# Performance work log

Measured on AMD Instinct MI355X. Metric: run time of the kernel, lower is better.

The kernel has to match this reference:

```python
import jax, jax.numpy as jnp
import numpy as np

N_NODES = 50000
N_EDGES = 300000
F_IN, HID, N_CLS = 256, 256, 128


def _glorot_linear(key, fan_in, fan_out):
    # torch.nn.Linear-style uniform init, kaiming bound 1/sqrt(fan_in)
    s = 1.0 / np.sqrt(fan_in)
    return jax.random.uniform(key, (fan_in, fan_out), jnp.float32, -s, s)


def setup_inputs() -> dict:
    key = jax.random.key(0)
    ks = jax.random.split(key, 8)
    x = jax.random.normal(ks[0], (N_NODES, F_IN), jnp.float32)
    edge_index = jax.random.randint(ks[1], (2, N_EDGES), 0, N_NODES, dtype=jnp.int32)
    return {
        "x": x,
        "edge_index": edge_index,
        "W1": _glorot_linear(ks[2], F_IN, HID), "b1": jnp.zeros((HID,), jnp.float32),
        "W2": _glorot_linear(ks[3], HID, HID),  "b2": jnp.zeros((HID,), jnp.float32),
        "W3": _glorot_linear(ks[4], HID, HID),  "b3": jnp.zeros((HID,), jnp.float32),
        "W4": _glorot_linear(ks[5], HID, N_CLS), "b4": jnp.zeros((N_CLS,), jnp.float32),
    }


def _gcn_conv(x, W, b, src, dst, norm, n):
    # x' = D^{-1/2} (A + I) D^{-1/2} X W + b   (PyG GCNConv default)
    h = x @ W                                  # [N, out]
    msg = h[src] * norm[:, None]               # gather + edge scaling  [E', out]
    return jax.ops.segment_sum(msg, dst, num_segments=n) + b


def reference(x, edge_index, W1, b1, W2, b2, W3, b3, W4, b4):
    n = x.shape[0]
    loops = jnp.arange(n, dtype=edge_index.dtype)
    src = jnp.concatenate([edge_index[0], loops])  # add self-loops
    dst = jnp.concatenate([edge_index[1], loops])
    # symmetric normalization: deg over target nodes (unit edge weights)
    deg = jax.ops.segment_sum(jnp.ones_like(dst, jnp.float32), dst, num_segments=n)
    dis = jnp.where(deg > 0, jax.lax.rsqrt(jnp.maximum(deg, 1.0)), 0.0)
    norm = dis[src] * dis[dst]                     # [E']

    h = jax.nn.relu(_gcn_conv(x, W1, b1, src, dst, norm, n))
    h = jax.nn.relu(_gcn_conv(h, W2, b2, src, dst, norm, n))
    h = jax.nn.relu(_gcn_conv(h, W3, b3, src, dst, norm, n))
    h = _gcn_conv(h, W4, b4, src, dst, norm, n)    # [N, C]

    # global_add_pool with batch == zeros -> single-graph sum pool
    pooled = jnp.sum(h, axis=0, keepdims=True)     # [1, C]
    return (pooled, jax.nn.log_softmax(pooled, axis=1))
```

## Files before the change

### kernel.cpp

```cpp
#include <hip/hip_runtime.h>


typedef __attribute__((ext_vector_type(8))) short short8;
typedef __attribute__((ext_vector_type(8))) signed char schar8;
typedef __attribute__((ext_vector_type(4))) float float4v;

__device__ __forceinline__ unsigned short f2b(float f) {
    unsigned int u = __builtin_bit_cast(unsigned int, f);
    u += 0x7fffu + ((u >> 16) & 1u);
    return (unsigned short)(u >> 16);
}
__device__ __forceinline__ float b2f(unsigned short b) {
    unsigned int u = ((unsigned int)b) << 16;
    return __builtin_bit_cast(float, u);
}

__global__ void zero_convert_kernel(int* __restrict__ cnt, float* __restrict__ tsum,
                                    float* __restrict__ accbuf,
                                    const float* __restrict__ W1, const float* __restrict__ W2,
                                    const float* __restrict__ W3, unsigned short* __restrict__ Wt1,
                                    unsigned short* __restrict__ Wt2, unsigned short* __restrict__ Wt3,
                                    const float* __restrict__ x, unsigned short* __restrict__ xb,
                                    int N, int nb) {
    int t = threadIdx.x;
    int b = blockIdx.x;
    if (b < nb) {
        int i = b * 256 + t;
        if (i < N) { cnt[i] = 0; tsum[i] = 0.f; }
        if (b == 0) accbuf[t] = 0.f;
    } else if (b < nb + 768) {
        int bb = b - nb;
        int w = bb >> 8;
        int n = bb & 255;
        const float* W = (w == 0) ? W1 : (w == 1) ? W2 : W3;
        unsigned short* Wt = (w == 0) ? Wt1 : (w == 1) ? Wt2 : Wt3;
        Wt[n * 256 + t] = f2b(W[t * 256 + n]);
    } else {
        size_t base = ((size_t)(b - nb - 768) * 256 + t) * 8;
        if (base < (size_t)N * 256) {
            float4 lo = *(const float4*)&x[base];
            float4 hi = *(const float4*)&x[base + 4];
            uint4 o;
            o.x = (unsigned int)f2b(lo.x) | ((unsigned int)f2b(lo.y) << 16);
            o.y = (unsigned int)f2b(lo.z) | ((unsigned int)f2b(lo.w) << 16);
            o.z = (unsigned int)f2b(hi.x) | ((unsigned int)f2b(hi.y) << 16);
            o.w = (unsigned int)f2b(hi.z) | ((unsigned int)f2b(hi.w) << 16);
            *(uint4*)&xb[base] = o;
        }
    }
}

__global__ void count_kernel(const int* __restrict__ dst, int* __restrict__ cnt, int E) {
    int i = blockIdx.x * blockDim.x + threadIdx.x;
    if (i < E) atomicAdd(&cnt[dst[i]], 1);
}

__global__ void blocksum_kernel(const int* __restrict__ cnt, int* __restrict__ bsum, int N) {
    __shared__ int s[256];
    int t = threadIdx.x;
    int i = blockIdx.x * 256 + t;
    s[t] = (i < N) ? cnt[i] : 0;
    __syncthreads();
    for (int d = 128; d > 0; d >>= 1) {
        if (t < d) s[t] += s[t + d];
        __syncthreads();
    }
    if (t == 0) bsum[blockIdx.x] = s[0];
}

__global__ void finalize_kernel(const int* __restrict__ cnt, const int* __restrict__ bsum,
                                int* __restrict__ offs, int* __restrict__ cursor,
                                float* __restrict__ dis, int N, int E, int nb) {
    __shared__ int bs[256];
    __shared__ int s[256];
    int t = threadIdx.x;
    bs[t] = (t < nb) ? bsum[t] : 0;
    __syncthreads();
    for (int d = 1; d < 256; d <<= 1) {
        int x = (t >= d) ? bs[t - d] : 0;
        __syncthreads();
        bs[t] += x;
        __syncthreads();
    }
    int blockoff = (blockIdx.x == 0) ? 0 : bs[blockIdx.x - 1];
    int i = blockIdx.x * 256 + t;
    int c = (i < N) ? cnt[i] : 0;
    s[t] = c;
    __syncthreads();
    for (int d = 1; d < 256; d <<= 1) {
        int x = (t >= d) ? s[t - d] : 0;
        __syncthreads();
        s[t] += x;
        __syncthreads();
    }
    if (i < N) {
        int ex = blockoff + s[t] - c;
        offs[i] = ex;
        cursor[i] = ex;
        dis[i] = rsqrtf((float)(c + 1));
    }
    if (blockIdx.x == 0 && t == 0) offs[N] = E;
}

__global__ void scatter_outsum_kernel(const int* __restrict__ src, const int* __restrict__ dst,
                                      const float* __restrict__ dis, int* __restrict__ cursor,
                                      int* __restrict__ csr_src, float* __restrict__ csr_nrm,
                                      float* __restrict__ tsum, int E) {
    int i = blockIdx.x * blockDim.x + threadIdx.x;
    if (i < E) {
        int s = src[i], d = dst[i];
        float dd = dis[d];
        int pos = atomicAdd(&cursor[d], 1);
        csr_src[pos] = s;
        csr_nrm[pos] = dis[s] * dd;
        atomicAdd(&tsum[s], dd);
    }
}

__global__ __launch_bounds__(256, 5) void gemm_bf16_kernel(
        const unsigned short* __restrict__ Ab, const unsigned short* __restrict__ Wt,
        signed char* __restrict__ C8, float* __restrict__ Ts, int M) {
    __shared__ unsigned short As[64 * 64];
    __shared__ unsigned short Bs[128 * 64];
    const int tid = threadIdx.x;
    const int lane = tid & 63;
    const int wave = tid >> 6;
    const int l15 = lane & 15;
    const int quad = lane >> 4;
    const int wm = wave & 1;
    const int wn = wave >> 1;

    const int bid = blockIdx.x;
    const int grp = bid >> 4;
    const int ii = bid & 15;
    const int xv = grp * 8 + (ii & 7);
    const int yv = ii >> 3;
    const int m0 = xv * 64;
    const int n0 = yv * 128;
    if (m0 >= M) return;

    float4v acc[2][4] = {};

    const int lrow = lane >> 3;
    const int lslot = (lane & 7) ^ lrow;

    const unsigned short* Bt = Wt + (size_t)n0 * 256;

    for (int kk = 0; kk < 256; kk += 64) {
#pragma unroll
        for (int i = 0; i < 2; i++) {
            int r0 = wave * 16 + i * 8;
            int gm = m0 + r0 + lrow;
            if (gm >= M) gm = M - 1;
            const unsigned short* gp = &Ab[(size_t)gm * 256 + kk + lslot * 8];
            __builtin_amdgcn_global_load_lds(
                (const __attribute__((address_space(1))) unsigned int*)gp,
                (__attribute__((address_space(3))) unsigned int*)&As[r0 * 64],
                16, 0, 0);
        }
#pragma unroll
        for (int i = 0; i < 4; i++) {
            int r0 = wave * 32 + i * 8;
            const unsigned short* gp = &Bt[(size_t)(r0 + lrow) * 256 + kk + lslot * 8];
            __builtin_amdgcn_global_load_lds(
                (const __attribute__((address_space(1))) unsigned int*)gp,
                (__attribute__((address_space(3))) unsigned int*)&Bs[r0 * 64],
                16, 0, 0);
        }
        __syncthreads();
#pragma unroll
        for (int ks = 0; ks < 64; ks += 32) {
            const int sl = (ks >> 3) + quad;
            short8 af[2], bf[4];
#pragma unroll
            for (int mi = 0; mi < 2; mi++) {
                int row = wm * 32 + mi * 16 + l15;
                af[mi] = *(const short8*)&As[row * 64 + 8 * (sl ^ (row & 7))];
            }
#pragma unroll
            for (int nj = 0; nj < 4; nj++) {
                int row = wn * 64 + nj * 16 + l15;
                bf[nj] = *(const short8*)&Bs[row * 64 + 8 * (sl ^ (row & 7))];
            }
#pragma unroll
            for (int mi = 0; mi < 2; mi++)
#pragma unroll
                for (int nj = 0; nj < 4; nj++)
                    acc[mi][nj] = __builtin_amdgcn_mfma_f32_16x16x32_bf16(
                        af[mi], bf[nj], acc[mi][nj], 0, 0, 0);
        }
        __syncthreads();
    }

    float* pmax = (float*)As;
    float* pinv = (float*)&As[512];
#pragma unroll
    for (int mi = 0; mi < 2; mi++) {
#pragma unroll
        for (int r = 0; r < 4; r++) {
            float m = fabsf(acc[mi][0][r]);
            m = fmaxf(m, fabsf(acc[mi][1][r]));
            m = fmaxf(m, fabsf(acc[mi][2][r]));
            m = fmaxf(m, fabsf(acc[mi][3][r]));
            m = fmaxf(m, __shfl_xor(m, 1));
            m = fmaxf(m, __shfl_xor(m, 2));
            m = fmaxf(m, __shfl_xor(m, 4));
            m = fmaxf(m, __shfl_xor(m, 8));
            if (l15 == 0) pmax[(wm * 32 + mi * 16 + quad * 4 + r) * 2 + wn] = m;
        }
    }
    __syncthreads();
    if (tid < 64) {
        float m = fmaxf(pmax[tid * 2], pmax[tid * 2 + 1]);
        int grow = m0 + tid;
        if (grow < M) Ts[(size_t)grow * 2 + yv] = m * (1.f / 127.f);
        pinv[tid] = (m > 0.f) ? 127.f / m : 0.f;
    }
    __syncthreads();
#pragma unroll
    for (int mi = 0; mi < 2; mi++) {
#pragma unroll
        for (int r = 0; r < 4; r++) {
            int lr = wm * 32 + mi * 16 + quad * 4 + r;
            float inv = pinv[lr];
            int row = m0 + lr;
            if (row < M) {
#pragma unroll
                for (int nj = 0; nj < 4; nj++) {
                    int col = n0 + wn * 64 + nj * 16 + l15;
                    C8[(size_t)row * 256 + col] =
                        (signed char)__float2int_rn(acc[mi][nj][r] * inv);
                }
            }
        }
    }
}

template <int RELU>
__global__ __launch_bounds__(256) void agg_bf16_kernel(
        const signed char* __restrict__ T8, const float* __restrict__ Ts,
        const float* __restrict__ bias,
        const int* __restrict__ offs, const int* __restrict__ csr_src,
        const float* __restrict__ csr_nrm, const float* __restrict__ dis,
        unsigned short* __restrict__ out, int N) {
    int hw = threadIdx.x >> 5;
    int l = threadIdx.x & 31;
    int v = blockIdx.x * 8 + hw;
    if (v >= N) return;
    int f8 = l * 8;
    int hh = l >> 4;
    int beg = offs[v], end = offs[v + 1];
    float dv = dis[v];
    float w = dv * dv * Ts[(size_t)v * 2 + hh];
    float a[8];
    {
        schar8 q = *(const schar8*)&T8[(size_t)v * 256 + f8];
#pragma unroll
        for (int i = 0; i < 8; i++) a[i] = w * (float)q[i];
    }
    int e = beg;
    for (; e + 4 <= end; e += 4) {
        int s0 = csr_src[e],     s1 = csr_src[e + 1];
        int s2 = csr_src[e + 2], s3 = csr_src[e + 3];
        float n0 = csr_nrm[e]     * Ts[(size_t)s0 * 2 + hh];
        float n1 = csr_nrm[e + 1] * Ts[(size_t)s1 * 2 + hh];
        float n2 = csr_nrm[e + 2] * Ts[(size_t)s2 * 2 + hh];
        float n3 = csr_nrm[e + 3] * Ts[(size_t)s3 * 2 + hh];
        schar8 h0 = *(const schar8*)&T8[(size_t)s0 * 256 + f8];
        schar8 h1 = *(const schar8*)&T8[(size_t)s1 * 256 + f8];
        schar8 h2 = *(const schar8*)&T8[(size_t)s2 * 256 + f8];
        schar8 h3 = *(const schar8*)&T8[(size_t)s3 * 256 + f8];
#pragma unroll
        for (int i = 0; i < 8; i++)
            a[i] += n0 * (float)h0[i] + n1 * (float)h1[i]
                  + n2 * (float)h2[i] + n3 * (float)h3[i];
    }
    for (; e < end; e++) {
        int s = csr_src[e];
        float nm = csr_nrm[e] * Ts[(size_t)s * 2 + hh];
        schar8 h = *(const schar8*)&T8[(size_t)s * 256 + f8];
#pragma unroll
        for (int i = 0; i < 8; i++) a[i] += nm * (float)h[i];
    }
    float4 bv0 = *(const float4*)&bias[f8];
    float4 bv1 = *(const float4*)&bias[f8 + 4];
    a[0] += bv0.x; a[1] += bv0.y; a[2] += bv0.z; a[3] += bv0.w;
    a[4] += bv1.x; a[5] += bv1.y; a[6] += bv1.z; a[7] += bv1.w;
    if (RELU) {
#pragma unroll
        for (int i = 0; i < 8; i++) a[i] = fmaxf(a[i], 0.f);
    }
    uint4 o;
    o.x = (unsigned int)f2b(a[0]) | ((unsigned int)f2b(a[1]) << 16);
    o.y = (unsigned int)f2b(a[2]) | ((unsigned int)f2b(a[3]) << 16);
    o.z = (unsigned int)f2b(a[4]) | ((unsigned int)f2b(a[5]) << 16);
    o.w = (unsigned int)f2b(a[6]) | ((unsigned int)f2b(a[7]) << 16);
    *(uint4*)&out[(size_t)v * 256 + f8] = o;
}

__global__ __launch_bounds__(256) void wpool_partial(
        const unsigned short* __restrict__ H, const float* __restrict__ dis,
        const float* __restrict__ tsum, float* __restrict__ partial, int N) {
    int tid = threadIdx.x;
    int f8 = (tid & 31) * 8;
    int rg = tid >> 5;
    float a[8] = {};
    for (int r = blockIdx.x * 8 + rg; r < N; r += gridDim.x * 8) {
        float s = dis[r] * (dis[r] + tsum[r]);
        short8 h = *(const short8*)&H[(size_t)r * 256 + f8];
#pragma unroll
        for (int i = 0; i < 8; i++) a[i] += s * b2f((unsigned short)h[i]);
    }
    __shared__ float red[8 * 256];
#pragma unroll
    for (int i = 0; i < 8; i++) red[rg * 256 + f8 + i] = a[i];
    __syncthreads();
    for (int s = 4; s > 0; s >>= 1) {
        if (rg < s) {
#pragma unroll
            for (int i = 0; i < 8; i++)
                red[rg * 256 + f8 + i] += red[(rg + s) * 256 + f8 + i];
        }
        __syncthreads();
    }
    partial[(size_t)blockIdx.x * 256 + tid] = red[tid];
}

__global__ void wpool_reduce(const float* __restrict__ partial, float* __restrict__ acc) {
    int f = threadIdx.x;
    int p0 = blockIdx.x * 32;
    float a = 0.f;
#pragma unroll
    for (int p = 0; p < 32; p++) a += partial[(size_t)(p0 + p) * 256 + f];
    atomicAdd(&acc[f], a);
}

__global__ void final_kernel(const float* __restrict__ acc, const float* __restrict__ W4,
                             const float* __restrict__ b4, float* __restrict__ out, int N) {
    __shared__ float red[128];
    int c = threadIdx.x;
    float p = (float)N * b4[c];
    for (int k = 0; k < 256; k++) p += acc[k] * W4[k * 128 + c];
    out[c] = p;
    red[c] = p;
    __syncthreads();
    for (int s = 64; s > 0; s >>= 1) {
        if (c < s) red[c] = fmaxf(red[c], red[c + s]);
        __syncthreads();
    }
    float m = red[0];
    __syncthreads();
    red[c] = expf(p - m);
    __syncthreads();
    for (int s = 64; s > 0; s >>= 1) {
        if (c < s) red[c] += red[c + s];
        __syncthreads();
    }
    float lse = m + logf(red[0]);
    out[128 + c] = p - lse;
}

extern "C" void kernel_launch(void* const* d_in, const int* in_sizes, int n_in,
                              void* d_out, int out_size, void* d_ws, size_t ws_size,
                              hipStream_t stream) {
    const float* x  = (const float*)d_in[0];
    const int*   ei = (const int*)d_in[1];
    const float* W1 = (const float*)d_in[2];
    const float* b1 = (const float*)d_in[3];
    const float* W2 = (const float*)d_in[4];
    const float* b2 = (const float*)d_in[5];
    const float* W3 = (const float*)d_in[6];
    const float* b3 = (const float*)d_in[7];
    const float* W4 = (const float*)d_in[8];
    const float* b4 = (const float*)d_in[9];

    const int N = in_sizes[0] / 256;
    const int E = in_sizes[1] / 2;
    const int* src = ei;
    const int* dst = ei + E;

    char* p = (char*)d_ws;
    auto alloc = [&](size_t bytes) {
        char* r = p;
        p += (bytes + 255) & ~(size_t)255;
        return r;
    };
    int*            cnt     = (int*)alloc((size_t)N * 4);
    int*            offs    = (int*)alloc((size_t)(N + 1) * 4);
    int*            cursor  = (int*)alloc((size_t)N * 4);
    float*          dis     = (float*)alloc((size_t)N * 4);
    float*          tsum    = (float*)alloc((size_t)N * 4);
    int*            bsum    = (int*)alloc(1024 * 4);
    int*            csr_src = (int*)alloc((size_t)E * 4);
    float*          csr_nrm = (float*)alloc((size_t)E * 4);
    unsigned short* Wt1     = (unsigned short*)alloc(256 * 256 * 2);
    unsigned short* Wt2     = (unsigned short*)alloc(256 * 256 * 2);
    unsigned short* Wt3     = (unsigned short*)alloc(256 * 256 * 2);
    unsigned short* xb      = (unsigned short*)alloc((size_t)N * 256 * 2);
    signed char*    T8      = (signed char*)alloc((size_t)N * 256);
    float*          Ts      = (float*)alloc((size_t)N * 2 * 4);
    unsigned short* Abuf    = (unsigned short*)alloc((size_t)N * 256 * 2);
    float*          partial = (float*)alloc((size_t)1024 * 256 * 4);
    float*          accbuf  = (float*)alloc(256 * 4);

    int eb = (E + 255) / 256;
    int nb = (N + 255) / 256;
    int ncvt = (N * 32 + 255) / 256;
    zero_convert_kernel<<<nb + 768 + ncvt, 256, 0, stream>>>(
        cnt, tsum, accbuf, W1, W2, W3, Wt1, Wt2, Wt3, x, xb, N, nb);
    count_kernel<<<eb, 256, 0, stream>>>(dst, cnt, E);
    blocksum_kernel<<<nb, 256, 0, stream>>>(cnt, bsum, N);
    finalize_kernel<<<nb, 256, 0, stream>>>(cnt, bsum, offs, cursor, dis, N, E, nb);
    scatter_outsum_kernel<<<eb, 256, 0, stream>>>(src, dst, dis, cursor, csr_src,
                                                  csr_nrm, tsum, E);

    int mtiles = (N + 63) / 64;
    int ggrid = ((mtiles + 7) / 8) * 16;
    int ab = (N + 7) / 8;
    gemm_bf16_kernel<<<ggrid, 256, 0, stream>>>(xb, Wt1, T8, Ts, N);
    agg_bf16_kernel<1><<<ab, 256, 0, stream>>>(T8, Ts, b1, offs, csr_src, csr_nrm, dis, Abuf, N);
    gemm_bf16_kernel<<<ggrid, 256, 0, stream>>>(Abuf, Wt2, T8, Ts, N);
    agg_bf16_kernel<1><<<ab, 256, 0, stream>>>(T8, Ts, b2, offs, csr_src, csr_nrm, dis, Abuf, N);
    gemm_bf16_kernel<<<ggrid, 256, 0, stream>>>(Abuf, Wt3, T8, Ts, N);
    agg_bf16_kernel<1><<<ab, 256, 0, stream>>>(T8, Ts, b3, offs, csr_src, csr_nrm, dis, Abuf, N);

    wpool_partial<<<1024, 256, 0, stream>>>(Abuf, dis, tsum, partial, N);
    wpool_reduce<<<32, 256, 0, stream>>>(partial, accbuf);
    final_kernel<<<1, 128, 0, stream>>>(accbuf, W4, b4, (float*)d_out, N);
}
```

Before: 294.2 us.

## Double-buffer GEMM LDS tiles with K-step 32 to overlap loads and MFMA

```diff
diff --git a/kernel.cpp b/kernel.cpp
--- a/kernel.cpp
+++ b/kernel.cpp
@@ -120,8 +120,8 @@
 __global__ __launch_bounds__(256, 5) void gemm_bf16_kernel(
         const unsigned short* __restrict__ Ab, const unsigned short* __restrict__ Wt,
         signed char* __restrict__ C8, float* __restrict__ Ts, int M) {
-    __shared__ unsigned short As[64 * 64];
-    __shared__ unsigned short Bs[128 * 64];
+    __shared__ unsigned short As[2 * 64 * 32];
+    __shared__ unsigned short Bs[2 * 128 * 32];
     const int tid = threadIdx.x;
     const int lane = tid & 63;
     const int wave = tid >> 6;
@@ -141,56 +141,63 @@
 
     float4v acc[2][4] = {};
 
-    const int lrow = lane >> 3;
-    const int lslot = (lane & 7) ^ lrow;
+    const int srow = lane >> 2;
+    const int sslot = (lane & 3) ^ ((lane >> 3) & 3);
 
     const unsigned short* Bt = Wt + (size_t)n0 * 256;
 
-    for (int kk = 0; kk < 256; kk += 64) {
-#pragma unroll
-        for (int i = 0; i < 2; i++) {
-            int r0 = wave * 16 + i * 8;
-            int gm = m0 + r0 + lrow;
-            if (gm >= M) gm = M - 1;
-            const unsigned short* gp = &Ab[(size_t)gm * 256 + kk + lslot * 8];
-            __builtin_amdgcn_global_load_lds(
-                (const __attribute__((address_space(1))) unsigned int*)gp,
-                (__attribute__((address_space(3))) unsigned int*)&As[r0 * 64],
-                16, 0, 0);
-        }
-#pragma unroll
-        for (int i = 0; i < 4; i++) {
-            int r0 = wave * 32 + i * 8;
-            const unsigned short* gp = &Bt[(size_t)(r0 + lrow) * 256 + kk + lslot * 8];
-            __builtin_amdgcn_global_load_lds(
-                (const __attribute__((address_space(1))) unsigned int*)gp,
-                (__attribute__((address_space(3))) unsigned int*)&Bs[r0 * 64],
-                16, 0, 0);
-        }
-        __syncthreads();
-#pragma unroll
-        for (int ks = 0; ks < 64; ks += 32) {
-            const int sl = (ks >> 3) + quad;
-            short8 af[2], bf[4];
-#pragma unroll
-            for (int mi = 0; mi < 2; mi++) {
-                int row = wm * 32 + mi * 16 + l15;
-                af[mi] = *(const short8*)&As[row * 64 + 8 * (sl ^ (row & 7))];
-            }
-#pragma unroll
-            for (int nj = 0; nj < 4; nj++) {
-                int row = wn * 64 + nj * 16 + l15;
-                bf[nj] = *(const short8*)&Bs[row * 64 + 8 * (sl ^ (row & 7))];
-            }
-#pragma unroll
-            for (int mi = 0; mi < 2; mi++)
-#pragma unroll
-                for (int nj = 0; nj < 4; nj++)
-                    acc[mi][nj] = __builtin_amdgcn_mfma_f32_16x16x32_bf16(
-                        af[mi], bf[nj], acc[mi][nj], 0, 0, 0);
-        }
-        __syncthreads();
-    }
+#define GSTAGE(buf, kk)                                                             \
+    {                                                                               \
+        {                                                                           \
+            int r0 = wave * 16;                                                     \
+            int gm = m0 + r0 + srow;                                                \
+            if (gm >= M) gm = M - 1;                                                \
+            const unsigned short* gp = &Ab[(size_t)gm * 256 + (kk) + sslot * 8];    \
+            __builtin_amdgcn_global_load_lds(                                       \
+                (const __attribute__((address_space(1))) unsigned int*)gp,          \
+                (__attribute__((address_space(3))) unsigned int*)&As[(buf) * 2048 + r0 * 32], \
+                16, 0, 0);                                                          \
+        }                                                                           \
+        _Pragma("unroll") for (int i_ = 0; i_ < 2; i_++) {                          \
+            int r0 = wave * 32 + i_ * 16;                                           \
+            const unsigned short* gp = &Bt[(size_t)(r0 + srow) * 256 + (kk) + sslot * 8]; \
+            __builtin_amdgcn_global_load_lds(                                       \
+                (const __attribute__((address_space(1))) unsigned int*)gp,          \
+                (__attribute__((address_space(3))) unsigned int*)&Bs[(buf) * 4096 + r0 * 32], \
+                16, 0, 0);                                                          \
+        }                                                                           \
+    }
+
+    GSTAGE(0, 0);
+    __syncthreads();
+    int cur = 0;
+#pragma unroll
+    for (int s = 0; s < 8; ++s) {
+        if (s < 7) GSTAGE(cur ^ 1, (s + 1) * 32);
+        __builtin_amdgcn_sched_barrier(0);
+        const unsigned short* Ac = &As[cur * 2048];
+        const unsigned short* Bc = &Bs[cur * 4096];
+        short8 af[2], bf[4];
+#pragma unroll
+        for (int mi = 0; mi < 2; mi++) {
+            int row = wm * 32 + mi * 16 + l15;
+            af[mi] = *(const short8*)&Ac[row * 32 + 8 * (quad ^ ((row >> 1) & 3))];
+        }
+#pragma unroll
+        for (int nj = 0; nj < 4; nj++) {
+            int row = wn * 64 + nj * 16 + l15;
+            bf[nj] = *(const short8*)&Bc[row * 32 + 8 * (quad ^ ((row >> 1) & 3))];
+        }
+#pragma unroll
+        for (int mi = 0; mi < 2; mi++)
+#pragma unroll
+            for (int nj = 0; nj < 4; nj++)
+                acc[mi][nj] = __builtin_amdgcn_mfma_f32_16x16x32_bf16(
+                    af[mi], bf[nj], acc[mi][nj], 0, 0, 0);
+        __syncthreads();
+        cur ^= 1;
+    }
+#undef GSTAGE
 
     float* pmax = (float*)As;
     float* pinv = (float*)&As[512];
```

New measurement: 297.8 us. Within noise of the previous version (+1.2%).

## Widen GEMM tile to full 256 columns with a single per-row int8 scale

Applied to the files above, without the earlier changes.

```diff
diff --git a/kernel.cpp b/kernel.cpp
--- a/kernel.cpp
+++ b/kernel.cpp
@@ -117,34 +117,24 @@
     }
 }
 
-__global__ __launch_bounds__(256, 5) void gemm_bf16_kernel(
+__global__ __launch_bounds__(256, 4) void gemm_bf16_kernel(
         const unsigned short* __restrict__ Ab, const unsigned short* __restrict__ Wt,
         signed char* __restrict__ C8, float* __restrict__ Ts, int M) {
     __shared__ unsigned short As[64 * 64];
-    __shared__ unsigned short Bs[128 * 64];
+    __shared__ unsigned short Bs[256 * 64];
     const int tid = threadIdx.x;
     const int lane = tid & 63;
     const int wave = tid >> 6;
     const int l15 = lane & 15;
     const int quad = lane >> 4;
-    const int wm = wave & 1;
-    const int wn = wave >> 1;
-
-    const int bid = blockIdx.x;
-    const int grp = bid >> 4;
-    const int ii = bid & 15;
-    const int xv = grp * 8 + (ii & 7);
-    const int yv = ii >> 3;
-    const int m0 = xv * 64;
-    const int n0 = yv * 128;
+    const int wn = wave;
+    const int m0 = blockIdx.x * 64;
     if (m0 >= M) return;
 
-    float4v acc[2][4] = {};
+    float4v acc[4][4] = {};
 
     const int lrow = lane >> 3;
     const int lslot = (lane & 7) ^ lrow;
-
-    const unsigned short* Bt = Wt + (size_t)n0 * 256;
 
     for (int kk = 0; kk < 256; kk += 64) {
 #pragma unroll
@@ -159,9 +149,9 @@
                 16, 0, 0);
         }
 #pragma unroll
-        for (int i = 0; i < 4; i++) {
-            int r0 = wave * 32 + i * 8;
-            const unsigned short* gp = &Bt[(size_t)(r0 + lrow) * 256 + kk + lslot * 8];
+        for (int i = 0; i < 8; i++) {
+            int r0 = wave * 64 + i * 8;
+            const unsigned short* gp = &Wt[(size_t)(r0 + lrow) * 256 + kk + lslot * 8];
             __builtin_amdgcn_global_load_lds(
                 (const __attribute__((address_space(1))) unsigned int*)gp,
                 (__attribute__((address_space(3))) unsigned int*)&Bs[r0 * 64],
@@ -171,10 +161,10 @@
 #pragma unroll
         for (int ks = 0; ks < 64; ks += 32) {
             const int sl = (ks >> 3) + quad;
-            short8 af[2], bf[4];
-#pragma unroll
-            for (int mi = 0; mi < 2; mi++) {
-                int row = wm * 32 + mi * 16 + l15;
+            short8 af[4], bf[4];
+#pragma unroll
+            for (int mi = 0; mi < 4; mi++) {
+                int row = mi * 16 + l15;
                 af[mi] = *(const short8*)&As[row * 64 + 8 * (sl ^ (row & 7))];
             }
 #pragma unroll
@@ -183,7 +173,7 @@
                 bf[nj] = *(const short8*)&Bs[row * 64 + 8 * (sl ^ (row & 7))];
             }
 #pragma unroll
-            for (int mi = 0; mi < 2; mi++)
+            for (int mi = 0; mi < 4; mi++)
 #pragma unroll
                 for (int nj = 0; nj < 4; nj++)
                     acc[mi][nj] = __builtin_amdgcn_mfma_f32_16x16x32_bf16(
@@ -195,7 +185,7 @@
     float* pmax = (float*)As;
     float* pinv = (float*)&As[512];
 #pragma unroll
-    for (int mi = 0; mi < 2; mi++) {
+    for (int mi = 0; mi < 4; mi++) {
 #pragma unroll
         for (int r = 0; r < 4; r++) {
             float m = fabsf(acc[mi][0][r]);
@@ -206,28 +196,29 @@
             m = fmaxf(m, __shfl_xor(m, 2));
             m = fmaxf(m, __shfl_xor(m, 4));
             m = fmaxf(m, __shfl_xor(m, 8));
-            if (l15 == 0) pmax[(wm * 32 + mi * 16 + quad * 4 + r) * 2 + wn] = m;
+            if (l15 == 0) pmax[(mi * 16 + quad * 4 + r) * 4 + wn] = m;
         }
     }
     __syncthreads();
     if (tid < 64) {
-        float m = fmaxf(pmax[tid * 2], pmax[tid * 2 + 1]);
+        float m = fmaxf(fmaxf(pmax[tid * 4], pmax[tid * 4 + 1]),
+                        fmaxf(pmax[tid * 4 + 2], pmax[tid * 4 + 3]));
         int grow = m0 + tid;
-        if (grow < M) Ts[(size_t)grow * 2 + yv] = m * (1.f / 127.f);
+        if (grow < M) Ts[grow] = m * (1.f / 127.f);
         pinv[tid] = (m > 0.f) ? 127.f / m : 0.f;
     }
     __syncthreads();
 #pragma unroll
-    for (int mi = 0; mi < 2; mi++) {
+    for (int mi = 0; mi < 4; mi++) {
 #pragma unroll
         for (int r = 0; r < 4; r++) {
-            int lr = wm * 32 + mi * 16 + quad * 4 + r;
+            int lr = mi * 16 + quad * 4 + r;
             float inv = pinv[lr];
             int row = m0 + lr;
             if (row < M) {
 #pragma unroll
                 for (int nj = 0; nj < 4; nj++) {
-                    int col = n0 + wn * 64 + nj * 16 + l15;
+                    int col = wn * 64 + nj * 16 + l15;
                     C8[(size_t)row * 256 + col] =
                         (signed char)__float2int_rn(acc[mi][nj][r] * inv);
                 }
@@ -248,10 +239,9 @@
     int v = blockIdx.x * 8 + hw;
     if (v >= N) return;
     int f8 = l * 8;
-    int hh = l >> 4;
     int beg = offs[v], end = offs[v + 1];
     float dv = dis[v];
-    float w = dv * dv * Ts[(size_t)v * 2 + hh];
+    float w = dv * dv * Ts[v];
     float a[8];
     {
         schar8 q = *(const schar8*)&T8[(size_t)v * 256 + f8];
@@ -262,10 +252,10 @@
     for (; e + 4 <= end; e += 4) {
         int s0 = csr_src[e],     s1 = csr_src[e + 1];
         int s2 = csr_src[e + 2], s3 = csr_src[e + 3];
-        float n0 = csr_nrm[e]     * Ts[(size_t)s0 * 2 + hh];
-        float n1 = csr_nrm[e + 1] * Ts[(size_t)s1 * 2 + hh];
-        float n2 = csr_nrm[e + 2] * Ts[(size_t)s2 * 2 + hh];
-        float n3 = csr_nrm[e + 3] * Ts[(size_t)s3 * 2 + hh];
+        float n0 = csr_nrm[e]     * Ts[s0];
+        float n1 = csr_nrm[e + 1] * Ts[s1];
+        float n2 = csr_nrm[e + 2] * Ts[s2];
+        float n3 = csr_nrm[e + 3] * Ts[s3];
         schar8 h0 = *(const schar8*)&T8[(size_t)s0 * 256 + f8];
         schar8 h1 = *(const schar8*)&T8[(size_t)s1 * 256 + f8];
         schar8 h2 = *(const schar8*)&T8[(size_t)s2 * 256 + f8];
@@ -277,7 +267,7 @@
     }
     for (; e < end; e++) {
         int s = csr_src[e];
-        float nm = csr_nrm[e] * Ts[(size_t)s * 2 + hh];
+        float nm = csr_nrm[e] * Ts[s];
         schar8 h = *(const schar8*)&T8[(size_t)s * 256 + f8];
 #pragma unroll
         for (int i = 0; i < 8; i++) a[i] += nm * (float)h[i];
@@ -398,7 +388,7 @@
     unsigned short* Wt3     = (unsigned short*)alloc(256 * 256 * 2);
     unsigned short* xb      = (unsigned short*)alloc((size_t)N * 256 * 2);
     signed char*    T8      = (signed char*)alloc((size_t)N * 256);
-    float*          Ts      = (float*)alloc((size_t)N * 2 * 4);
+    float*          Ts      = (float*)alloc((size_t)N * 4);
     unsigned short* Abuf    = (unsigned short*)alloc((size_t)N * 256 * 2);
     float*          partial = (float*)alloc((size_t)1024 * 256 * 4);
     float*          accbuf  = (float*)alloc(256 * 4);
@@ -414,8 +404,7 @@
     scatter_outsum_kernel<<<eb, 256, 0, stream>>>(src, dst, dis, cursor, csr_src,
                                                   csr_nrm, tsum, E);
 
-    int mtiles = (N + 63) / 64;
-    int ggrid = ((mtiles + 7) / 8) * 16;
+    int ggrid = (N + 63) / 64;
     int ab = (N + 7) / 8;
     gemm_bf16_kernel<<<ggrid, 256, 0, stream>>>(xb, Wt1, T8, Ts, N);
     agg_bf16_kernel<1><<<ab, 256, 0, stream>>>(T8, Ts, b1, offs, csr_src, csr_nrm, dis, Abuf, N);
```

Result: no change. 295.6 us, median of 2 (+0.5%).
